# Optimization experiments

Hardware: AMD Instinct MI355X
Metric: run time of the kernel (lower is better)

Reference implementation:

```python
import jax, jax.numpy as jnp
import numpy as np

N_NODES = 50000
N_EDGES = 800000


def setup_inputs() -> dict:
    key = jax.random.key(0)
    k1, k2, k3, k4 = jax.random.split(key, 4)
    x = jax.random.normal(k1, (N_NODES, 100), dtype=jnp.float32)
    edge_index = jax.random.randint(k2, (2, N_EDGES), 0, N_NODES, dtype=jnp.int64)
    W1 = jax.random.normal(k3, (100, 128), dtype=jnp.float32) * 0.1
    b1 = jnp.zeros((128,), dtype=jnp.float32)
    W2 = jax.random.normal(k4, (128, 64), dtype=jnp.float32) * 0.1
    b2 = jnp.zeros((64,), dtype=jnp.float32)
    return {"x": x, "edge_index": edge_index, "W1": W1, "b1": b1, "W2": W2, "b2": b2}


def _gcn_norm(edge_index, n_nodes):
    # PyG GCNConv default: add self-loops, then symmetric normalization
    row, col = edge_index[0], edge_index[1]
    loop = jnp.arange(n_nodes, dtype=row.dtype)
    row = jnp.concatenate([row, loop])
    col = jnp.concatenate([col, loop])
    deg = jax.ops.segment_sum(jnp.ones_like(col, dtype=jnp.float32), col,
                              num_segments=n_nodes)
    dinv = jnp.where(deg > 0, jax.lax.rsqrt(deg), 0.0)
    norm = dinv[row] * dinv[col]  # [E + N]
    return row, col, norm


def _gcn_conv(x, W, b, row, col, norm, n_nodes):
    h = x @ W                       # [N, out] linear transform first (PyG order)
    msg = norm[:, None] * h[row]    # gather + scale over edges
    agg = jax.ops.segment_sum(msg, col, num_segments=n_nodes)  # scatter-add
    return agg + b


def reference(x, edge_index, W1, b1, W2, b2):
    n = x.shape[0]
    row, col, norm = _gcn_norm(edge_index, n)
    h = _gcn_conv(x, W1, b1, row, col, norm, n)
    h = jax.nn.relu(h)
    out = _gcn_conv(h, W2, b2, row, col, norm, n)
    return out
```

## Files before the change

kernel.cpp:

```cpp
#include <hip/hip_runtime.h>
#include <hip/hip_fp16.h>

#define DIV_UP(a,b) (((a)+(b)-1)/(b))

typedef _Float16 half8 __attribute__((ext_vector_type(8)));
typedef float f32x4 __attribute__((ext_vector_type(4)));

#define BUK_BITS 8
#define BUK_SIZE 256
#define BUK_CAP  6144
#define CSR_CAP  8192
#define MAXBUK   256
#define NBLK_BUCKET 256
#define CHUNK_MAX 3136

#define SWZ(row, colh) ((colh) ^ (((row) & 7) << 3))


__device__ __forceinline__ int edge_at(const void* ei, int mode64, int idx) {
  if (mode64) return (int)((const long long*)ei)[idx];
  return ((const int*)ei)[idx];
}

__global__ __launch_bounds__(256) void k_init(const int* __restrict__ ei32,
                                              int* __restrict__ mode,
                                              int* __restrict__ bcur, int nbuk,
                                              const float* __restrict__ W1,
                                              const float* __restrict__ W2,
                                              _Float16* __restrict__ Wt1,
                                              _Float16* __restrict__ Wt2) {
  int t = threadIdx.x;
  if (blockIdx.x == 0) {
    if (t < 64) {
      int v = ei32[2 * t + 1];
      unsigned long long b = __ballot(v == 0);
      if (t == 0) *mode = (b == ~0ull) ? 1 : 0;
    }
    if (t < nbuk) bcur[t] = t * BUK_CAP;
  } else {
    int i = (blockIdx.x - 1) * 256 + t;
    if (i < 128 * 128) {
      int nn = i >> 7, k = i & 127;
      Wt1[i] = (k < 100) ? (_Float16)W1[k * 128 + nn] : (_Float16)0.f;
    } else {
      int j = i - 128 * 128;
      int nn = j >> 7, k = j & 127;
      Wt2[j] = (_Float16)W2[k * 64 + nn];
    }
  }
}

__global__ __launch_bounds__(256) void k_bucket(const void* __restrict__ ei,
                                                const int* __restrict__ mode,
                                                int* __restrict__ bcur,
                                                unsigned int* __restrict__ recs,
                                                int E, int nbuk) {
  __shared__ unsigned int lrec[CHUNK_MAX];
  __shared__ unsigned int sorted[CHUNK_MAX];
  __shared__ int hist[MAXBUK], lofs[MAXBUK], gbase[MAXBUK], cur[MAXBUK];

  const int chunk = DIV_UP(E, gridDim.x);
  const int e0 = blockIdx.x * chunk;
  const int cnt = min(E, e0 + chunk) - e0;
  if (cnt <= 0) return;

  for (int i = threadIdx.x; i < nbuk; i += 256) hist[i] = 0;
  __syncthreads();

  const int m = *mode;
  for (int i = threadIdx.x; i < cnt; i += 256) {
    int r = edge_at(ei, m, e0 + i);
    int c = edge_at(ei, m, E + e0 + i);
    unsigned int rec = ((unsigned)c << 16) | (unsigned)r;
    lrec[i] = rec;
    atomicAdd(&hist[c >> BUK_BITS], 1);
  }
  __syncthreads();

  if (threadIdx.x == 0) {
    int run = 0;
    for (int b = 0; b < nbuk; ++b) { lofs[b] = run; run += hist[b]; }
  }
  __syncthreads();
  for (int b = threadIdx.x; b < nbuk; b += 256) {
    gbase[b] = atomicAdd(&bcur[b], hist[b]);
    cur[b] = lofs[b];
  }
  __syncthreads();

  for (int i = threadIdx.x; i < cnt; i += 256) {
    unsigned int rec = lrec[i];
    int b = rec >> (16 + BUK_BITS);
    int p = atomicAdd(&cur[b], 1);
    sorted[p] = rec;
  }
  __syncthreads();

  for (int i = threadIdx.x; i < cnt; i += 256) {
    unsigned int rec = sorted[i];
    int b = rec >> (16 + BUK_BITS);
    recs[gbase[b] + i - lofs[b]] = rec;
  }
}

__global__ __launch_bounds__(256) void k_bdeg_fill(const int* __restrict__ bcur,
                                                   const unsigned int* __restrict__ recs,
                                                   float* __restrict__ dinv,
                                                   int2* __restrict__ rowinfo,
                                                   unsigned short* __restrict__ csr,
                                                   int n) {
  __shared__ int h[BUK_SIZE];
  __shared__ int psum[BUK_SIZE];
  __shared__ int curs[BUK_SIZE];
  __shared__ unsigned short lcsr[CSR_CAP];

  const int b = blockIdx.x, tid = threadIdx.x;
  const int base = b * BUK_CAP;
  const int cnt = bcur[b] - base;
  const int n0 = b << BUK_BITS;
  const int nn = min(BUK_SIZE, n - n0);

  h[tid] = 0;
  __syncthreads();
  for (int i = tid; i < cnt; i += 256)
    atomicAdd(&h[(int)(recs[base + i] >> 16) - n0], 1);
  __syncthreads();

  const int deg = h[tid];
  const int plen = (deg + 7) & ~7;
  psum[tid] = plen;
  __syncthreads();
#pragma unroll
  for (int off2 = 1; off2 < 256; off2 <<= 1) {
    int v = (tid >= off2) ? psum[tid - off2] : 0;
    __syncthreads();
    psum[tid] += v;
    __syncthreads();
  }
  const int excl = psum[tid] - plen;
  const int ptot = psum[255];

  if (tid < nn) {
    rowinfo[n0 + tid] = make_int2(b * CSR_CAP + excl, plen);
    dinv[n0 + tid] = rsqrtf((float)deg + 1.0f);
    curs[tid] = excl;
  }
  for (int i = tid; i < ptot; i += 256) lcsr[i] = (unsigned short)n;
  __syncthreads();

  for (int i = tid; i < cnt; i += 256) {
    unsigned int rec = recs[base + i];
    int cl = (int)(rec >> 16) - n0;
    int p = atomicAdd(&curs[cl], 1);
    lcsr[p] = (unsigned short)(rec & 0xFFFFu);
  }
  __syncthreads();
  for (int i = tid; i < ptot; i += 256) csr[b * CSR_CAP + i] = lcsr[i];
}

__global__ __launch_bounds__(256) void k_convx(const float4* __restrict__ x4,
                                               const float* __restrict__ dinv,
                                               uint2* __restrict__ xh4,
                                               uint2* __restrict__ thh2,
                                               int n, int total4) {
  int i = blockIdx.x * 256 + threadIdx.x;
  if (i < total4) {
    int node = i / 25;
    int lane = i - node * 25;
    float d = dinv[node];
    float4 v = x4[i];
    union { uint2 u; __half2 h[2]; } p;
    p.h[0] = __halves2half2(__float2half_rn(d * v.x), __float2half_rn(d * v.y));
    p.h[1] = __halves2half2(__float2half_rn(d * v.z), __float2half_rn(d * v.w));
    xh4[(node << 5) + lane] = p.u;
  } else {
    int s = i - total4;
    if (s < 32) xh4[(n << 5) + s] = make_uint2(0u, 0u);
    else if (s < 48) thh2[n * 16 + (s - 32)] = make_uint2(0u, 0u);
  }
}

__device__ __forceinline__ float4 h4_to_f4(uint2 u) {
  union { uint2 u; __half2 h[2]; } p; p.u = u;
  float2 a = __half22float2(p.h[0]);
  float2 b = __half22float2(p.h[1]);
  return make_float4(a.x, a.y, b.x, b.y);
}
__device__ __forceinline__ void acc_add(float4& acc, float4 a) {
  acc.x += a.x; acc.y += a.y; acc.z += a.z; acc.w += a.w;
}

__global__ __launch_bounds__(256) void k_pull1(const int2* __restrict__ rowinfo,
                                               const unsigned short* __restrict__ csr,
                                               const uint2* __restrict__ xh4,
                                               const float* __restrict__ dinv,
                                               uint2* __restrict__ aggh4, int n) {
  int g = threadIdx.x / 25;
  int lane = threadIdx.x - g * 25;
  if (g >= 10) return;
  int node = blockIdx.x * 10 + g;
  if (node >= n) return;

  float4 acc = h4_to_f4(xh4[(node << 5) + lane]);
  int2 ri = rowinfo[node];
  int beg = ri.x, end = ri.x + ri.y;
  for (int j = beg; j < end; j += 8) {
    uint4 cw = *(const uint4*)&csr[j];
    int r0 = cw.x & 0xFFFF, r1 = cw.x >> 16;
    int r2 = cw.y & 0xFFFF, r3 = cw.y >> 16;
    int r4 = cw.z & 0xFFFF, r5 = cw.z >> 16;
    int r6 = cw.w & 0xFFFF, r7 = cw.w >> 16;
    float4 t0 = h4_to_f4(xh4[(r0 << 5) + lane]);
    float4 t1 = h4_to_f4(xh4[(r1 << 5) + lane]);
    float4 t2 = h4_to_f4(xh4[(r2 << 5) + lane]);
    float4 t3 = h4_to_f4(xh4[(r3 << 5) + lane]);
    float4 t4 = h4_to_f4(xh4[(r4 << 5) + lane]);
    float4 t5 = h4_to_f4(xh4[(r5 << 5) + lane]);
    float4 t6 = h4_to_f4(xh4[(r6 << 5) + lane]);
    float4 t7 = h4_to_f4(xh4[(r7 << 5) + lane]);
    acc_add(acc, t0); acc_add(acc, t1); acc_add(acc, t2); acc_add(acc, t3);
    acc_add(acc, t4); acc_add(acc, t5); acc_add(acc, t6); acc_add(acc, t7);
  }
  float d = dinv[node];
  union { uint2 u; __half2 h[2]; } p;
  p.h[0] = __halves2half2(__float2half_rn(d * acc.x), __float2half_rn(d * acc.y));
  p.h[1] = __halves2half2(__float2half_rn(d * acc.z), __float2half_rn(d * acc.w));
  aggh4[node * 32 + lane] = p.u;
  if (lane < 7) aggh4[node * 32 + 25 + lane] = make_uint2(0u, 0u);
}

__global__ __launch_bounds__(256) void k_pull2(const int2* __restrict__ rowinfo,
                                               const unsigned short* __restrict__ csr,
                                               const uint4* __restrict__ th4,
                                               const float* __restrict__ dinv,
                                               const float4* __restrict__ b2_4,
                                               float4* __restrict__ out4, int n) {
  int g = threadIdx.x >> 3;
  int lane = threadIdx.x & 7;
  int node = blockIdx.x * 32 + g;
  if (node >= n) return;

  uint4 sv = th4[(node << 3) + lane];
  float4 acc0 = h4_to_f4(make_uint2(sv.x, sv.y));
  float4 acc1 = h4_to_f4(make_uint2(sv.z, sv.w));

  int2 ri = rowinfo[node];
  int beg = ri.x, end = ri.x + ri.y;
  for (int j = beg; j < end; j += 8) {
    uint4 cw = *(const uint4*)&csr[j];
    int r0 = cw.x & 0xFFFF, r1 = cw.x >> 16;
    int r2 = cw.y & 0xFFFF, r3 = cw.y >> 16;
    int r4 = cw.z & 0xFFFF, r5 = cw.z >> 16;
    int r6 = cw.w & 0xFFFF, r7 = cw.w >> 16;
    uint4 u0 = th4[(r0 << 3) + lane];
    uint4 u1 = th4[(r1 << 3) + lane];
    uint4 u2 = th4[(r2 << 3) + lane];
    uint4 u3 = th4[(r3 << 3) + lane];
    uint4 u4 = th4[(r4 << 3) + lane];
    uint4 u5 = th4[(r5 << 3) + lane];
    uint4 u6 = th4[(r6 << 3) + lane];
    uint4 u7 = th4[(r7 << 3) + lane];
    acc_add(acc0, h4_to_f4(make_uint2(u0.x, u0.y)));
    acc_add(acc1, h4_to_f4(make_uint2(u0.z, u0.w)));
    acc_add(acc0, h4_to_f4(make_uint2(u1.x, u1.y)));
    acc_add(acc1, h4_to_f4(make_uint2(u1.z, u1.w)));
    acc_add(acc0, h4_to_f4(make_uint2(u2.x, u2.y)));
    acc_add(acc1, h4_to_f4(make_uint2(u2.z, u2.w)));
    acc_add(acc0, h4_to_f4(make_uint2(u3.x, u3.y)));
    acc_add(acc1, h4_to_f4(make_uint2(u3.z, u3.w)));
    acc_add(acc0, h4_to_f4(make_uint2(u4.x, u4.y)));
    acc_add(acc1, h4_to_f4(make_uint2(u4.z, u4.w)));
    acc_add(acc0, h4_to_f4(make_uint2(u5.x, u5.y)));
    acc_add(acc1, h4_to_f4(make_uint2(u5.z, u5.w)));
    acc_add(acc0, h4_to_f4(make_uint2(u6.x, u6.y)));
    acc_add(acc1, h4_to_f4(make_uint2(u6.z, u6.w)));
    acc_add(acc0, h4_to_f4(make_uint2(u7.x, u7.y)));
    acc_add(acc1, h4_to_f4(make_uint2(u7.z, u7.w)));
  }
  float d = dinv[node];
  float4 bb0 = b2_4[lane * 2], bb1 = b2_4[lane * 2 + 1];
  out4[node * 16 + lane * 2]     = make_float4(d * acc0.x + bb0.x, d * acc0.y + bb0.y,
                                               d * acc0.z + bb0.z, d * acc0.w + bb0.w);
  out4[node * 16 + lane * 2 + 1] = make_float4(d * acc1.x + bb1.x, d * acc1.y + bb1.y,
                                               d * acc1.z + bb1.z, d * acc1.w + bb1.w);
}

__global__ __launch_bounds__(256, 2) void k_gemmf(const _Float16* __restrict__ A,
                                                  const _Float16* __restrict__ Wt1,
                                                  const float* __restrict__ b1,
                                                  const _Float16* __restrict__ Wt2,
                                                  const float* __restrict__ dinv,
                                                  _Float16* __restrict__ thh, int n) {
  __shared__ __align__(16) _Float16 lds[4][16 * 128];
  const int wid = threadIdx.x >> 6;
  const int lane = threadIdx.x & 63;
  const int lr = lane & 15;
  const int lk = lane >> 4;
  _Float16* myl = lds[wid];

  half8 B1[8][4];
#pragma unroll
  for (int nt = 0; nt < 8; ++nt)
#pragma unroll
    for (int ks = 0; ks < 4; ++ks)
      B1[nt][ks] = *(const half8*)&Wt1[(nt * 16 + lr) * 128 + ks * 32 + lk * 8];
  float bs[8];
#pragma unroll
  for (int nt = 0; nt < 8; ++nt) bs[nt] = b1[nt * 16 + lr];

  const int nstrips = (n + 15) >> 4;
  for (int s = blockIdx.x * 4 + wid; s < nstrips; s += gridDim.x * 4) {
    const int arow = s * 16 + lr;
    half8 a[4];
#pragma unroll
    for (int ks = 0; ks < 4; ++ks)
      a[ks] = (arow < n) ? *(const half8*)&A[(size_t)arow * 128 + ks * 32 + lk * 8]
                         : half8{0, 0, 0, 0, 0, 0, 0, 0};
    f32x4 acc[8];
#pragma unroll
    for (int nt = 0; nt < 8; ++nt) acc[nt] = f32x4{0.f, 0.f, 0.f, 0.f};
#pragma unroll
    for (int ks = 0; ks < 4; ++ks)
#pragma unroll
      for (int nt = 0; nt < 8; ++nt)
        acc[nt] = __builtin_amdgcn_mfma_f32_16x16x32_f16(a[ks], B1[nt][ks], acc[nt], 0, 0, 0);

#pragma unroll
    for (int r = 0; r < 4; ++r) {
      int row = lk * 4 + r;
#pragma unroll
      for (int nt = 0; nt < 8; ++nt)
        myl[row * 128 + SWZ(row, nt * 16 + lr)] =
            (_Float16)fmaxf(acc[nt][r] + bs[nt], 0.f);
    }

    half8 B2[4][4];
#pragma unroll
    for (int nt = 0; nt < 4; ++nt)
#pragma unroll
      for (int ks = 0; ks < 4; ++ks)
        B2[nt][ks] = *(const half8*)&Wt2[(nt * 16 + lr) * 128 + ks * 32 + lk * 8];

    half8 a2[4];
#pragma unroll
    for (int ks = 0; ks < 4; ++ks)
      a2[ks] = *(const half8*)&myl[lr * 128 + SWZ(lr, ks * 32 + lk * 8)];

    f32x4 acc2[4];
#pragma unroll
    for (int nt = 0; nt < 4; ++nt) acc2[nt] = f32x4{0.f, 0.f, 0.f, 0.f};
#pragma unroll
    for (int ks = 0; ks < 4; ++ks)
#pragma unroll
      for (int nt = 0; nt < 4; ++nt)
        acc2[nt] = __builtin_amdgcn_mfma_f32_16x16x32_f16(a2[ks], B2[nt][ks], acc2[nt], 0, 0, 0);

    const int rb = s * 16 + lk * 4;
    float sc[4];
    if (rb + 3 < n) {
      const float4 dv = *(const float4*)&dinv[rb];
      sc[0] = dv.x; sc[1] = dv.y; sc[2] = dv.z; sc[3] = dv.w;
    } else {
#pragma unroll
      for (int r = 0; r < 4; ++r) sc[r] = (rb + r < n) ? dinv[rb + r] : 0.f;
    }
#pragma unroll
    for (int r = 0; r < 4; ++r) {
      const int orow = rb + r;
      if (orow < n) {
#pragma unroll
        for (int nt = 0; nt < 4; ++nt)
          thh[(size_t)orow * 64 + nt * 16 + lr] = (_Float16)(acc2[nt][r] * sc[r]);
      }
    }
  }
}

extern "C" void kernel_launch(void* const* d_in, const int* in_sizes, int n_in,
                              void* d_out, int out_size, void* d_ws, size_t ws_size,
                              hipStream_t stream) {
  const float* x  = (const float*)d_in[0];
  const void*  ei = d_in[1];
  const float* W1 = (const float*)d_in[2];
  const float* b1 = (const float*)d_in[3];
  const float* W2 = (const float*)d_in[4];
  const float* b2 = (const float*)d_in[5];
  float* out = (float*)d_out;

  const int n = in_sizes[0] / 100;
  const int E = in_sizes[1] / 2;
  const int nbuk = DIV_UP(n, BUK_SIZE);

  char* ws = (char*)d_ws;
  size_t off = 0;
  auto alloc = [&](size_t bytes) { void* p = ws + off; off += (bytes + 15) & ~15ull; return p; };
  int*            mode     = (int*)   alloc(64 * 4);
  int*            bcur     = (int*)   alloc(MAXBUK * 4);
  float*          dinv     = (float*) alloc((size_t)n * 4);
  int2*           rowinfo  = (int2*)  alloc((size_t)n * 8);
  unsigned int*   recs     = (unsigned int*)alloc((size_t)nbuk * BUK_CAP * 4);
  unsigned short* csr      = (unsigned short*)alloc((size_t)nbuk * CSR_CAP * 2);
  _Float16*       xh       = (_Float16*)alloc((size_t)(n + 1) * 128 * 2);
  _Float16*       aggh     = (_Float16*)alloc((size_t)n * 128 * 2);
  _Float16*       thh      = (_Float16*)alloc((size_t)(n + 1) * 64 * 2);
  _Float16*       Wt1h     = (_Float16*)alloc(128 * 128 * 2);
  _Float16*       Wt2h     = (_Float16*)alloc(64 * 128 * 2);

  k_init<<<97, 256, 0, stream>>>((const int*)ei, mode, bcur, nbuk, W1, W2, Wt1h, Wt2h);
  k_bucket<<<NBLK_BUCKET, 256, 0, stream>>>(ei, mode, bcur, recs, E, nbuk);
  k_bdeg_fill<<<nbuk, 256, 0, stream>>>(bcur, recs, dinv, rowinfo, csr, n);

  const int total4 = n * 25;
  k_convx<<<DIV_UP(total4 + 48, 256), 256, 0, stream>>>((const float4*)x, dinv,
      (uint2*)xh, (uint2*)thh, n, total4);

  k_pull1<<<DIV_UP(n, 10), 256, 0, stream>>>(rowinfo, csr, (const uint2*)xh, dinv,
                                             (uint2*)aggh, n);
  const int nstrips = DIV_UP(n, 16);
  k_gemmf<<<DIV_UP(nstrips, 8), 256, 0, stream>>>(aggh, Wt1h, b1, Wt2h, dinv, thh, n);
  k_pull2<<<DIV_UP(n, 32), 256, 0, stream>>>(rowinfo, csr, (const uint4*)thh, dinv,
                                             (const float4*)b2, (float4*)out, n);
}
```

Before: 119.4 us.

## Split gather-aggregate feature columns into slices across blocks for cache locality

```diff
diff --git a/kernel.cpp b/kernel.cpp
--- a/kernel.cpp
+++ b/kernel.cpp
@@ -162,21 +162,24 @@
                                                const float* __restrict__ dinv,
                                                uint2* __restrict__ xh4,
                                                uint2* __restrict__ thh2,
-                                               int n, int total4) {
+                                               int n, int total) {
   int i = blockIdx.x * 256 + threadIdx.x;
-  if (i < total4) {
-    int node = i / 25;
-    int lane = i - node * 25;
-    float d = dinv[node];
-    float4 v = x4[i];
-    union { uint2 u; __half2 h[2]; } p;
-    p.h[0] = __halves2half2(__float2half_rn(d * v.x), __float2half_rn(d * v.y));
-    p.h[1] = __halves2half2(__float2half_rn(d * v.z), __float2half_rn(d * v.w));
-    xh4[(node << 5) + lane] = p.u;
+  if (i < total) {
+    int node = i >> 5;
+    int lane = i & 31;
+    if (node < n && lane < 25) {
+      float d = dinv[node];
+      float4 v = x4[node * 25 + lane];
+      union { uint2 u; __half2 h[2]; } p;
+      p.h[0] = __halves2half2(__float2half_rn(d * v.x), __float2half_rn(d * v.y));
+      p.h[1] = __halves2half2(__float2half_rn(d * v.z), __float2half_rn(d * v.w));
+      xh4[i] = p.u;
+    } else {
+      xh4[i] = make_uint2(0u, 0u);
+    }
   } else {
-    int s = i - total4;
-    if (s < 32) xh4[(n << 5) + s] = make_uint2(0u, 0u);
-    else if (s < 48) thh2[n * 16 + (s - 32)] = make_uint2(0u, 0u);
+    int s = i - total;
+    if (s < 16) thh2[n * 16 + s] = make_uint2(0u, 0u);
   }
 }
 
@@ -195,13 +198,15 @@
                                                const uint2* __restrict__ xh4,
                                                const float* __restrict__ dinv,
                                                uint2* __restrict__ aggh4, int n) {
-  int g = threadIdx.x / 25;
-  int lane = threadIdx.x - g * 25;
-  if (g >= 10) return;
-  int node = blockIdx.x * 10 + g;
+  const int b = blockIdx.x;
+  const int slice = (b & 7) >> 1;
+  const int g = ((b >> 3) << 1) + (b & 1);
+  const int node = g * 32 + (threadIdx.x >> 3);
+  const int lane = threadIdx.x & 7;
   if (node >= n) return;
-
-  float4 acc = h4_to_f4(xh4[(node << 5) + lane]);
+  const int so = slice * 8 + lane;
+
+  float4 acc = h4_to_f4(xh4[(node << 5) + so]);
   int2 ri = rowinfo[node];
   int beg = ri.x, end = ri.x + ri.y;
   for (int j = beg; j < end; j += 8) {
@@ -210,14 +215,14 @@
     int r2 = cw.y & 0xFFFF, r3 = cw.y >> 16;
     int r4 = cw.z & 0xFFFF, r5 = cw.z >> 16;
     int r6 = cw.w & 0xFFFF, r7 = cw.w >> 16;
-    float4 t0 = h4_to_f4(xh4[(r0 << 5) + lane]);
-    float4 t1 = h4_to_f4(xh4[(r1 << 5) + lane]);
-    float4 t2 = h4_to_f4(xh4[(r2 << 5) + lane]);
-    float4 t3 = h4_to_f4(xh4[(r3 << 5) + lane]);
-    float4 t4 = h4_to_f4(xh4[(r4 << 5) + lane]);
-    float4 t5 = h4_to_f4(xh4[(r5 << 5) + lane]);
-    float4 t6 = h4_to_f4(xh4[(r6 << 5) + lane]);
-    float4 t7 = h4_to_f4(xh4[(r7 << 5) + lane]);
+    float4 t0 = h4_to_f4(xh4[(r0 << 5) + so]);
+    float4 t1 = h4_to_f4(xh4[(r1 << 5) + so]);
+    float4 t2 = h4_to_f4(xh4[(r2 << 5) + so]);
+    float4 t3 = h4_to_f4(xh4[(r3 << 5) + so]);
+    float4 t4 = h4_to_f4(xh4[(r4 << 5) + so]);
+    float4 t5 = h4_to_f4(xh4[(r5 << 5) + so]);
+    float4 t6 = h4_to_f4(xh4[(r6 << 5) + so]);
+    float4 t7 = h4_to_f4(xh4[(r7 << 5) + so]);
     acc_add(acc, t0); acc_add(acc, t1); acc_add(acc, t2); acc_add(acc, t3);
     acc_add(acc, t4); acc_add(acc, t5); acc_add(acc, t6); acc_add(acc, t7);
   }
@@ -225,25 +230,24 @@
   union { uint2 u; __half2 h[2]; } p;
   p.h[0] = __halves2half2(__float2half_rn(d * acc.x), __float2half_rn(d * acc.y));
   p.h[1] = __halves2half2(__float2half_rn(d * acc.z), __float2half_rn(d * acc.w));
-  aggh4[node * 32 + lane] = p.u;
-  if (lane < 7) aggh4[node * 32 + 25 + lane] = make_uint2(0u, 0u);
+  aggh4[(node << 5) + so] = p.u;
 }
 
 __global__ __launch_bounds__(256) void k_pull2(const int2* __restrict__ rowinfo,
                                                const unsigned short* __restrict__ csr,
-                                               const uint4* __restrict__ th4,
+                                               const uint2* __restrict__ th2,
                                                const float* __restrict__ dinv,
                                                const float4* __restrict__ b2_4,
                                                float4* __restrict__ out4, int n) {
-  int g = threadIdx.x >> 3;
-  int lane = threadIdx.x & 7;
-  int node = blockIdx.x * 32 + g;
+  const int b = blockIdx.x;
+  const int slice = (b & 7) >> 2;
+  const int g = ((b >> 3) << 2) + (b & 3);
+  const int node = g * 32 + (threadIdx.x >> 3);
+  const int lane = threadIdx.x & 7;
   if (node >= n) return;
-
-  uint4 sv = th4[(node << 3) + lane];
-  float4 acc0 = h4_to_f4(make_uint2(sv.x, sv.y));
-  float4 acc1 = h4_to_f4(make_uint2(sv.z, sv.w));
-
+  const int so = slice * 8 + lane;
+
+  float4 acc = h4_to_f4(th2[(node << 4) + so]);
   int2 ri = rowinfo[node];
   int beg = ri.x, end = ri.x + ri.y;
   for (int j = beg; j < end; j += 8) {
@@ -252,37 +256,21 @@
     int r2 = cw.y & 0xFFFF, r3 = cw.y >> 16;
     int r4 = cw.z & 0xFFFF, r5 = cw.z >> 16;
     int r6 = cw.w & 0xFFFF, r7 = cw.w >> 16;
-    uint4 u0 = th4[(r0 << 3) + lane];
-    uint4 u1 = th4[(r1 << 3) + lane];
-    uint4 u2 = th4[(r2 << 3) + lane];
-    uint4 u3 = th4[(r3 << 3) + lane];
-    uint4 u4 = th4[(r4 << 3) + lane];
-    uint4 u5 = th4[(r5 << 3) + lane];
-    uint4 u6 = th4[(r6 << 3) + lane];
-    uint4 u7 = th4[(r7 << 3) + lane];
-    acc_add(acc0, h4_to_f4(make_uint2(u0.x, u0.y)));
-    acc_add(acc1, h4_to_f4(make_uint2(u0.z, u0.w)));
-    acc_add(acc0, h4_to_f4(make_uint2(u1.x, u1.y)));
-    acc_add(acc1, h4_to_f4(make_uint2(u1.z, u1.w)));
-    acc_add(acc0, h4_to_f4(make_uint2(u2.x, u2.y)));
-    acc_add(acc1, h4_to_f4(make_uint2(u2.z, u2.w)));
-    acc_add(acc0, h4_to_f4(make_uint2(u3.x, u3.y)));
-    acc_add(acc1, h4_to_f4(make_uint2(u3.z, u3.w)));
-    acc_add(acc0, h4_to_f4(make_uint2(u4.x, u4.y)));
-    acc_add(acc1, h4_to_f4(make_uint2(u4.z, u4.w)));
-    acc_add(acc0, h4_to_f4(make_uint2(u5.x, u5.y)));
-    acc_add(acc1, h4_to_f4(make_uint2(u5.z, u5.w)));
-    acc_add(acc0, h4_to_f4(make_uint2(u6.x, u6.y)));
-    acc_add(acc1, h4_to_f4(make_uint2(u6.z, u6.w)));
-    acc_add(acc0, h4_to_f4(make_uint2(u7.x, u7.y)));
-    acc_add(acc1, h4_to_f4(make_uint2(u7.z, u7.w)));
+    float4 t0 = h4_to_f4(th2[(r0 << 4) + so]);
+    float4 t1 = h4_to_f4(th2[(r1 << 4) + so]);
+    float4 t2 = h4_to_f4(th2[(r2 << 4) + so]);
+    float4 t3 = h4_to_f4(th2[(r3 << 4) + so]);
+    float4 t4 = h4_to_f4(th2[(r4 << 4) + so]);
+    float4 t5 = h4_to_f4(th2[(r5 << 4) + so]);
+    float4 t6 = h4_to_f4(th2[(r6 << 4) + so]);
+    float4 t7 = h4_to_f4(th2[(r7 << 4) + so]);
+    acc_add(acc, t0); acc_add(acc, t1); acc_add(acc, t2); acc_add(acc, t3);
+    acc_add(acc, t4); acc_add(acc, t5); acc_add(acc, t6); acc_add(acc, t7);
   }
   float d = dinv[node];
-  float4 bb0 = b2_4[lane * 2], bb1 = b2_4[lane * 2 + 1];
-  out4[node * 16 + lane * 2]     = make_float4(d * acc0.x + bb0.x, d * acc0.y + bb0.y,
-                                               d * acc0.z + bb0.z, d * acc0.w + bb0.w);
-  out4[node * 16 + lane * 2 + 1] = make_float4(d * acc1.x + bb1.x, d * acc1.y + bb1.y,
-                                               d * acc1.z + bb1.z, d * acc1.w + bb1.w);
+  float4 bb = b2_4[so];
+  out4[(node << 4) + so] = make_float4(d * acc.x + bb.x, d * acc.y + bb.y,
+                                       d * acc.z + bb.z, d * acc.w + bb.w);
 }
 
 __global__ __launch_bounds__(256, 2) void k_gemmf(const _Float16* __restrict__ A,
@@ -410,14 +398,16 @@
   k_bucket<<<NBLK_BUCKET, 256, 0, stream>>>(ei, mode, bcur, recs, E, nbuk);
   k_bdeg_fill<<<nbuk, 256, 0, stream>>>(bcur, recs, dinv, rowinfo, csr, n);
 
-  const int total4 = n * 25;
-  k_convx<<<DIV_UP(total4 + 48, 256), 256, 0, stream>>>((const float4*)x, dinv,
-      (uint2*)xh, (uint2*)thh, n, total4);
-
-  k_pull1<<<DIV_UP(n, 10), 256, 0, stream>>>(rowinfo, csr, (const uint2*)xh, dinv,
-                                             (uint2*)aggh, n);
+  const int total = (n + 1) * 32;
+  k_convx<<<DIV_UP(total + 16, 256), 256, 0, stream>>>((const float4*)x, dinv,
+      (uint2*)xh, (uint2*)thh, n, total);
+
+  const int ngroups = DIV_UP(n, 32);
+  k_pull1<<<DIV_UP(ngroups, 2) * 8, 256, 0, stream>>>(rowinfo, csr, (const uint2*)xh,
+                                                      dinv, (uint2*)aggh, n);
   const int nstrips = DIV_UP(n, 16);
   k_gemmf<<<DIV_UP(nstrips, 8), 256, 0, stream>>>(aggh, Wt1h, b1, Wt2h, dinv, thh, n);
-  k_pull2<<<DIV_UP(n, 32), 256, 0, stream>>>(rowinfo, csr, (const uint4*)thh, dinv,
-                                             (const float4*)b2, (float4*)out, n);
-}
+  k_pull2<<<DIV_UP(ngroups, 4) * 8, 256, 0, stream>>>(rowinfo, csr, (const uint2*)thh,
+                                                      dinv, (const float4*)b2,
+                                                      (float4*)out, n);
+}
```

After: 120.7 us. Within noise of the previous version (+1.1%).

## Fuse x conversion into bucket-degree kernel and prefetch CSR indices in pull loops

Applied to the files above, without the earlier changes.

```diff
diff --git a/kernel.cpp b/kernel.cpp
--- a/kernel.cpp
+++ b/kernel.cpp
@@ -105,9 +105,12 @@
 
 __global__ __launch_bounds__(256) void k_bdeg_fill(const int* __restrict__ bcur,
                                                    const unsigned int* __restrict__ recs,
+                                                   const float4* __restrict__ x4,
                                                    float* __restrict__ dinv,
                                                    int2* __restrict__ rowinfo,
                                                    unsigned short* __restrict__ csr,
+                                                   uint2* __restrict__ xh4,
+                                                   uint2* __restrict__ thh2,
                                                    int n) {
   __shared__ int h[BUK_SIZE];
   __shared__ int psum[BUK_SIZE];
@@ -156,27 +159,24 @@
   }
   __syncthreads();
   for (int i = tid; i < ptot; i += 256) csr[b * CSR_CAP + i] = lcsr[i];
-}
-
-__global__ __launch_bounds__(256) void k_convx(const float4* __restrict__ x4,
-                                               const float* __restrict__ dinv,
-                                               uint2* __restrict__ xh4,
-                                               uint2* __restrict__ thh2,
-                                               int n, int total4) {
-  int i = blockIdx.x * 256 + threadIdx.x;
-  if (i < total4) {
-    int node = i / 25;
-    int lane = i - node * 25;
-    float d = dinv[node];
-    float4 v = x4[i];
-    union { uint2 u; __half2 h[2]; } p;
-    p.h[0] = __halves2half2(__float2half_rn(d * v.x), __float2half_rn(d * v.y));
-    p.h[1] = __halves2half2(__float2half_rn(d * v.z), __float2half_rn(d * v.w));
-    xh4[(node << 5) + lane] = p.u;
-  } else {
-    int s = i - total4;
-    if (s < 32) xh4[(n << 5) + s] = make_uint2(0u, 0u);
-    else if (s < 48) thh2[n * 16 + (s - 32)] = make_uint2(0u, 0u);
+
+  for (int i = tid; i < nn * 32; i += 256) {
+    int nl = i >> 5, lane = i & 31;
+    int node = n0 + nl;
+    uint2 val = make_uint2(0u, 0u);
+    if (lane < 25) {
+      float d = rsqrtf((float)h[nl] + 1.0f);
+      float4 v = x4[node * 25 + lane];
+      union { uint2 u; __half2 hh[2]; } p;
+      p.hh[0] = __halves2half2(__float2half_rn(d * v.x), __float2half_rn(d * v.y));
+      p.hh[1] = __halves2half2(__float2half_rn(d * v.z), __float2half_rn(d * v.w));
+      val = p.u;
+    }
+    xh4[(node << 5) + lane] = val;
+  }
+  if (b == 0) {
+    if (tid < 32) xh4[(n << 5) + tid] = make_uint2(0u, 0u);
+    else if (tid < 48) thh2[(n << 4) + (tid - 32)] = make_uint2(0u, 0u);
   }
 }
 
@@ -204,29 +204,34 @@
   float4 acc = h4_to_f4(xh4[(node << 5) + lane]);
   int2 ri = rowinfo[node];
   int beg = ri.x, end = ri.x + ri.y;
-  for (int j = beg; j < end; j += 8) {
-    uint4 cw = *(const uint4*)&csr[j];
-    int r0 = cw.x & 0xFFFF, r1 = cw.x >> 16;
-    int r2 = cw.y & 0xFFFF, r3 = cw.y >> 16;
-    int r4 = cw.z & 0xFFFF, r5 = cw.z >> 16;
-    int r6 = cw.w & 0xFFFF, r7 = cw.w >> 16;
-    float4 t0 = h4_to_f4(xh4[(r0 << 5) + lane]);
-    float4 t1 = h4_to_f4(xh4[(r1 << 5) + lane]);
-    float4 t2 = h4_to_f4(xh4[(r2 << 5) + lane]);
-    float4 t3 = h4_to_f4(xh4[(r3 << 5) + lane]);
-    float4 t4 = h4_to_f4(xh4[(r4 << 5) + lane]);
-    float4 t5 = h4_to_f4(xh4[(r5 << 5) + lane]);
-    float4 t6 = h4_to_f4(xh4[(r6 << 5) + lane]);
-    float4 t7 = h4_to_f4(xh4[(r7 << 5) + lane]);
-    acc_add(acc, t0); acc_add(acc, t1); acc_add(acc, t2); acc_add(acc, t3);
-    acc_add(acc, t4); acc_add(acc, t5); acc_add(acc, t6); acc_add(acc, t7);
+  if (beg < end) {
+    uint4 cw = *(const uint4*)&csr[beg];
+    for (int j = beg; j < end; ) {
+      j += 8;
+      uint4 nx = (j < end) ? *(const uint4*)&csr[j] : cw;
+      int r0 = cw.x & 0xFFFF, r1 = cw.x >> 16;
+      int r2 = cw.y & 0xFFFF, r3 = cw.y >> 16;
+      int r4 = cw.z & 0xFFFF, r5 = cw.z >> 16;
+      int r6 = cw.w & 0xFFFF, r7 = cw.w >> 16;
+      float4 t0 = h4_to_f4(xh4[(r0 << 5) + lane]);
+      float4 t1 = h4_to_f4(xh4[(r1 << 5) + lane]);
+      float4 t2 = h4_to_f4(xh4[(r2 << 5) + lane]);
+      float4 t3 = h4_to_f4(xh4[(r3 << 5) + lane]);
+      float4 t4 = h4_to_f4(xh4[(r4 << 5) + lane]);
+      float4 t5 = h4_to_f4(xh4[(r5 << 5) + lane]);
+      float4 t6 = h4_to_f4(xh4[(r6 << 5) + lane]);
+      float4 t7 = h4_to_f4(xh4[(r7 << 5) + lane]);
+      acc_add(acc, t0); acc_add(acc, t1); acc_add(acc, t2); acc_add(acc, t3);
+      acc_add(acc, t4); acc_add(acc, t5); acc_add(acc, t6); acc_add(acc, t7);
+      cw = nx;
+    }
   }
   float d = dinv[node];
   union { uint2 u; __half2 h[2]; } p;
   p.h[0] = __halves2half2(__float2half_rn(d * acc.x), __float2half_rn(d * acc.y));
   p.h[1] = __halves2half2(__float2half_rn(d * acc.z), __float2half_rn(d * acc.w));
-  aggh4[node * 32 + lane] = p.u;
-  if (lane < 7) aggh4[node * 32 + 25 + lane] = make_uint2(0u, 0u);
+  aggh4[(node << 5) + lane] = p.u;
+  if (lane < 7) aggh4[(node << 5) + 25 + lane] = make_uint2(0u, 0u);
 }
 
 __global__ __launch_bounds__(256) void k_pull2(const int2* __restrict__ rowinfo,
@@ -246,43 +251,48 @@
 
   int2 ri = rowinfo[node];
   int beg = ri.x, end = ri.x + ri.y;
-  for (int j = beg; j < end; j += 8) {
-    uint4 cw = *(const uint4*)&csr[j];
-    int r0 = cw.x & 0xFFFF, r1 = cw.x >> 16;
-    int r2 = cw.y & 0xFFFF, r3 = cw.y >> 16;
-    int r4 = cw.z & 0xFFFF, r5 = cw.z >> 16;
-    int r6 = cw.w & 0xFFFF, r7 = cw.w >> 16;
-    uint4 u0 = th4[(r0 << 3) + lane];
-    uint4 u1 = th4[(r1 << 3) + lane];
-    uint4 u2 = th4[(r2 << 3) + lane];
-    uint4 u3 = th4[(r3 << 3) + lane];
-    uint4 u4 = th4[(r4 << 3) + lane];
-    uint4 u5 = th4[(r5 << 3) + lane];
-    uint4 u6 = th4[(r6 << 3) + lane];
-    uint4 u7 = th4[(r7 << 3) + lane];
-    acc_add(acc0, h4_to_f4(make_uint2(u0.x, u0.y)));
-    acc_add(acc1, h4_to_f4(make_uint2(u0.z, u0.w)));
-    acc_add(acc0, h4_to_f4(make_uint2(u1.x, u1.y)));
-    acc_add(acc1, h4_to_f4(make_uint2(u1.z, u1.w)));
-    acc_add(acc0, h4_to_f4(make_uint2(u2.x, u2.y)));
-    acc_add(acc1, h4_to_f4(make_uint2(u2.z, u2.w)));
-    acc_add(acc0, h4_to_f4(make_uint2(u3.x, u3.y)));
-    acc_add(acc1, h4_to_f4(make_uint2(u3.z, u3.w)));
-    acc_add(acc0, h4_to_f4(make_uint2(u4.x, u4.y)));
-    acc_add(acc1, h4_to_f4(make_uint2(u4.z, u4.w)));
-    acc_add(acc0, h4_to_f4(make_uint2(u5.x, u5.y)));
-    acc_add(acc1, h4_to_f4(make_uint2(u5.z, u5.w)));
-    acc_add(acc0, h4_to_f4(make_uint2(u6.x, u6.y)));
-    acc_add(acc1, h4_to_f4(make_uint2(u6.z, u6.w)));
-    acc_add(acc0, h4_to_f4(make_uint2(u7.x, u7.y)));
-    acc_add(acc1, h4_to_f4(make_uint2(u7.z, u7.w)));
+  if (beg < end) {
+    uint4 cw = *(const uint4*)&csr[beg];
+    for (int j = beg; j < end; ) {
+      j += 8;
+      uint4 nx = (j < end) ? *(const uint4*)&csr[j] : cw;
+      int r0 = cw.x & 0xFFFF, r1 = cw.x >> 16;
+      int r2 = cw.y & 0xFFFF, r3 = cw.y >> 16;
+      int r4 = cw.z & 0xFFFF, r5 = cw.z >> 16;
+      int r6 = cw.w & 0xFFFF, r7 = cw.w >> 16;
+      uint4 u0 = th4[(r0 << 3) + lane];
+      uint4 u1 = th4[(r1 << 3) + lane];
+      uint4 u2 = th4[(r2 << 3) + lane];
+      uint4 u3 = th4[(r3 << 3) + lane];
+      uint4 u4 = th4[(r4 << 3) + lane];
+      uint4 u5 = th4[(r5 << 3) + lane];
+      uint4 u6 = th4[(r6 << 3) + lane];
+      uint4 u7 = th4[(r7 << 3) + lane];
+      acc_add(acc0, h4_to_f4(make_uint2(u0.x, u0.y)));
+      acc_add(acc1, h4_to_f4(make_uint2(u0.z, u0.w)));
+      acc_add(acc0, h4_to_f4(make_uint2(u1.x, u1.y)));
+      acc_add(acc1, h4_to_f4(make_uint2(u1.z, u1.w)));
+      acc_add(acc0, h4_to_f4(make_uint2(u2.x, u2.y)));
+      acc_add(acc1, h4_to_f4(make_uint2(u2.z, u2.w)));
+      acc_add(acc0, h4_to_f4(make_uint2(u3.x, u3.y)));
+      acc_add(acc1, h4_to_f4(make_uint2(u3.z, u3.w)));
+      acc_add(acc0, h4_to_f4(make_uint2(u4.x, u4.y)));
+      acc_add(acc1, h4_to_f4(make_uint2(u4.z, u4.w)));
+      acc_add(acc0, h4_to_f4(make_uint2(u5.x, u5.y)));
+      acc_add(acc1, h4_to_f4(make_uint2(u5.z, u5.w)));
+      acc_add(acc0, h4_to_f4(make_uint2(u6.x, u6.y)));
+      acc_add(acc1, h4_to_f4(make_uint2(u6.z, u6.w)));
+      acc_add(acc0, h4_to_f4(make_uint2(u7.x, u7.y)));
+      acc_add(acc1, h4_to_f4(make_uint2(u7.z, u7.w)));
+      cw = nx;
+    }
   }
   float d = dinv[node];
   float4 bb0 = b2_4[lane * 2], bb1 = b2_4[lane * 2 + 1];
-  out4[node * 16 + lane * 2]     = make_float4(d * acc0.x + bb0.x, d * acc0.y + bb0.y,
-                                               d * acc0.z + bb0.z, d * acc0.w + bb0.w);
-  out4[node * 16 + lane * 2 + 1] = make_float4(d * acc1.x + bb1.x, d * acc1.y + bb1.y,
-                                               d * acc1.z + bb1.z, d * acc1.w + bb1.w);
+  out4[(node << 4) + lane * 2]     = make_float4(d * acc0.x + bb0.x, d * acc0.y + bb0.y,
+                                                 d * acc0.z + bb0.z, d * acc0.w + bb0.w);
+  out4[(node << 4) + lane * 2 + 1] = make_float4(d * acc1.x + bb1.x, d * acc1.y + bb1.y,
+                                                 d * acc1.z + bb1.z, d * acc1.w + bb1.w);
 }
 
 __global__ __launch_bounds__(256, 2) void k_gemmf(const _Float16* __restrict__ A,
@@ -408,11 +418,8 @@
 
   k_init<<<97, 256, 0, stream>>>((const int*)ei, mode, bcur, nbuk, W1, W2, Wt1h, Wt2h);
   k_bucket<<<NBLK_BUCKET, 256, 0, stream>>>(ei, mode, bcur, recs, E, nbuk);
-  k_bdeg_fill<<<nbuk, 256, 0, stream>>>(bcur, recs, dinv, rowinfo, csr, n);
-
-  const int total4 = n * 25;
-  k_convx<<<DIV_UP(total4 + 48, 256), 256, 0, stream>>>((const float4*)x, dinv,
-      (uint2*)xh, (uint2*)thh, n, total4);
+  k_bdeg_fill<<<nbuk, 256, 0, stream>>>(bcur, recs, (const float4*)x, dinv,
+                                        rowinfo, csr, (uint2*)xh, (uint2*)thh, n);
 
   k_pull1<<<DIV_UP(n, 10), 256, 0, stream>>>(rowinfo, csr, (const uint2*)xh, dinv,
                                              (uint2*)aggh, n);
```

Measured after the change: 139.3 us. +16.6%, slower.
